# Performance work log

Measured on AMD Instinct MI355X. Metric: run time of the kernel, lower is better.

The kernel has to match this reference:

```python
import jax, jax.numpy as jnp
import numpy as np

B, S, H = 32, 2048, 1024
A = 1024  # attention_hidden_size
EPS = 1e-5


def setup_inputs() -> dict:
    key = jax.random.key(0)
    ks = jax.random.split(key, 16)
    sc_h = 1.0 / np.sqrt(H)
    sc_a = 1.0 / np.sqrt(A)
    sc_2h = 1.0 / np.sqrt(2 * H)
    return {
        "seq_states": jax.random.normal(ks[0], (B, S, H), jnp.float32),
        "q_state": jax.random.normal(ks[1], (B, H), jnp.float32),
        "Wk": jax.random.uniform(ks[2], (H, A), jnp.float32, -sc_h, sc_h),
        "bk": jax.random.uniform(ks[3], (A,), jnp.float32, -sc_h, sc_h),
        "Wq": jax.random.uniform(ks[4], (H, A), jnp.float32, -sc_h, sc_h),
        "bq": jax.random.uniform(ks[5], (A,), jnp.float32, -sc_h, sc_h),
        "Wg": jax.random.uniform(ks[6], (A, A), jnp.float32, -sc_a, sc_a),
        "bg": jax.random.uniform(ks[7], (A,), jnp.float32, -sc_a, sc_a),
        "Ws": jax.random.uniform(ks[8], (A, 1), jnp.float32, -sc_a, sc_a),
        "bs": jax.random.uniform(ks[9], (1,), jnp.float32, -sc_a, sc_a),
        "Wo": jax.random.uniform(ks[10], (2 * H, H), jnp.float32, -sc_2h, sc_2h),
        "bo": jax.random.uniform(ks[11], (H,), jnp.float32, -sc_2h, sc_2h),
        "gamma": jnp.ones((H,), jnp.float32),
        "beta": jnp.zeros((H,), jnp.float32),
    }


def reference(seq_states, q_state, Wk, bk, Wq, bq, Wg, bg, Ws, bs, Wo, bo, gamma, beta):
    keys = jnp.einsum("bsh,ha->bsa", seq_states, Wk) + bk          # [B,S,A]
    query = (q_state @ Wq + bq)[:, None, :]                          # [B,1,A]
    alignment = jnp.tanh(keys + query)                               # [B,S,A]
    gate = jax.nn.sigmoid(jnp.einsum("bsa,ac->bsc", alignment, Wg) + bg)
    gated = alignment * gate                                         # dropout p=0.0 -> identity
    scores = jnp.einsum("bsa,ao->bso", gated, Ws)[..., 0] + bs[0]    # [B,S]
    weights = jax.nn.softmax(scores, axis=1)                         # [B,S]
    context = jnp.einsum("bs,bsh->bh", weights, seq_states)          # [B,H]
    fused_in = jnp.concatenate([context, q_state], axis=-1)          # [B,2H]
    pre = fused_in @ Wo + bo + q_state                               # residual
    mu = jnp.mean(pre, axis=-1, keepdims=True)
    var = jnp.var(pre, axis=-1, keepdims=True)
    fused = (pre - mu) * jax.lax.rsqrt(var + EPS) * gamma + beta
    return (fused, weights)
```

## Files before the change

kernel.cpp:

```cpp
#include <hip/hip_runtime.h>

typedef __attribute__((ext_vector_type(8))) short bf16x8;
typedef __attribute__((ext_vector_type(8))) unsigned short ushort8;
typedef __attribute__((ext_vector_type(4))) unsigned short ushortx4;
typedef __attribute__((ext_vector_type(4))) float f32x4;

#define BM 256
#define BN 256
#define BK 64

__device__ __forceinline__ unsigned short f2bf(float f) {
  union { float f; unsigned u; } c; c.f = f;
  return (unsigned short)((c.u + 0x7fffu + ((c.u >> 16) & 1u)) >> 16);
}
__device__ __forceinline__ float bf2f(unsigned short u) {
  union { unsigned u; float f; } c; c.u = ((unsigned)u) << 16;
  return c.f;
}
__device__ __forceinline__ float fast_tanh(float x) {
  float e = __expf(2.f * x);
  return 1.f - 2.f * __builtin_amdgcn_rcpf(e + 1.f);
}
__device__ __forceinline__ float fast_sigmoid(float x) {
  return __builtin_amdgcn_rcpf(1.f + __expf(-x));
}
__device__ __forceinline__ void gload16(const void* g, void* lds) {
  __builtin_amdgcn_global_load_lds(
      (const __attribute__((address_space(1))) unsigned int*)g,
      (__attribute__((address_space(3))) unsigned int*)lds, 16, 0, 0);
}
__device__ __forceinline__ void bar() {
  asm volatile("" ::: "memory");
  __builtin_amdgcn_s_barrier();
  asm volatile("" ::: "memory");
}
__device__ __forceinline__ void sb0() { __builtin_amdgcn_sched_barrier(0); }
template <int N> __device__ __forceinline__ void vlgkm() {
  if constexpr (N == 0) asm volatile("s_waitcnt lgkmcnt(0)" ::: "memory");
  else if constexpr (N == 4) asm volatile("s_waitcnt lgkmcnt(4)" ::: "memory");
  else if constexpr (N == 8) asm volatile("s_waitcnt lgkmcnt(8)" ::: "memory");
}
template <int N> __device__ __forceinline__ void vwait() {
  if constexpr (N < 0) {
  } else if constexpr (N == 2) asm volatile("s_waitcnt vmcnt(2)" ::: "memory");
  else if constexpr (N == 0) asm volatile("s_waitcnt vmcnt(0)" ::: "memory");
}

__device__ __forceinline__ void mfma16(const bf16x8 (&a)[4], const bf16x8 (&b)[4], int ro,
                                       f32x4 (&acc)[8][4]) {
  __builtin_amdgcn_s_setprio(1);
#pragma unroll
  for (int i = 0; i < 4; ++i)
#pragma unroll
    for (int n = 0; n < 4; ++n)
      acc[ro + i][n] =
          __builtin_amdgcn_mfma_f32_16x16x32_bf16(a[i], b[n], acc[ro + i][n], 0, 0, 0);
  __builtin_amdgcn_s_setprio(0);
}

template <bool ST, bool ST4, bool RD4, int W3, int W4>
__device__ __forceinline__ void ktile(
    const char* rAk0, const char* rAk1, const char* rBk1,
    const char* rAk0n, const char* rBk0n,
    char* dAn, char* dBn,
    char* dAc,
    const unsigned short* pA0, const unsigned short* pA1,
    const unsigned short* pB0, const unsigned short* pB1,
    int kN1, int kN2,
    bf16x8 (&aX)[4], bf16x8 (&aY)[4], bf16x8 (&b0)[4], bf16x8 (&b1)[4],
    f32x4 (&acc)[8][4]) {
  bar();
#pragma unroll
  for (int i = 0; i < 4; ++i) aY[i] = *(const bf16x8*)(rAk0 + 16384 + i * 2048);
  if (ST) { gload16(pB0 + kN1, dBn); gload16(pB1 + kN1, dBn + 8192); }
  vlgkm<4>(); sb0();
  mfma16(aX, b0, 0, acc);
  bar();
#pragma unroll
  for (int i = 0; i < 4; ++i) aX[i] = *(const bf16x8*)(rAk1 + i * 2048);
#pragma unroll
  for (int n = 0; n < 4; ++n)
    b1[n] = *(const bf16x8*)(rBk1 + (n >> 1) * 16384 + (n & 1) * 2048);
  if (ST) { gload16(pB0 + 32768 + kN1, dBn + 16384); gload16(pB1 + 32768 + kN1, dBn + 16384 + 8192); }
  vlgkm<8>(); sb0();
  mfma16(aY, b0, 4, acc);
  bar();
#pragma unroll
  for (int i = 0; i < 4; ++i) aY[i] = *(const bf16x8*)(rAk1 + 16384 + i * 2048);
  if (ST) { gload16(pA0 + 65536 + kN1, dAn + 16384); gload16(pA1 + 65536 + kN1, dAn + 16384 + 8192); }
  vlgkm<4>(); sb0();
  mfma16(aX, b1, 0, acc);
  vwait<W3>();
  bar();
  if (RD4) {
#pragma unroll
    for (int i = 0; i < 4; ++i) aX[i] = *(const bf16x8*)(rAk0n + i * 2048);
#pragma unroll
    for (int n = 0; n < 4; ++n)
      b0[n] = *(const bf16x8*)(rBk0n + (n >> 1) * 16384 + (n & 1) * 2048);
  }
  if (ST4) { gload16(pA0 + kN2, dAc); gload16(pA1 + kN2, dAc + 8192); }
  if (RD4) vlgkm<8>(); else vlgkm<0>();
  sb0();
  mfma16(aY, b1, 4, acc);
  vwait<W4>();
}

#define GEMM_SETUP_AND_PIPELINE(Ag, Bg)                                                    \
  int t = threadIdx.x, lane = t & 63, wave = t >> 6;                                       \
  int wr = wave >> 2, wc = wave & 3;                                                       \
  int sl0 = ((lane >> 4) ^ (lane & 7)) * 16;                                               \
  int sl1 = (((lane >> 4) + 4) ^ (lane & 7)) * 16;                                         \
  int aLane = (wr * 64 + (lane & 15)) * 128;                                               \
  int bLane = (wc * 32 + (lane & 15)) * 128;                                               \
  const char* rA0k0 = (const char*)As0 + aLane + sl0;                                      \
  const char* rA0k1 = (const char*)As0 + aLane + sl1;                                      \
  const char* rA1k0 = (const char*)As1 + aLane + sl0;                                      \
  const char* rA1k1 = (const char*)As1 + aLane + sl1;                                      \
  const char* rB0k0 = (const char*)Bs0 + bLane + sl0;                                      \
  const char* rB0k1 = (const char*)Bs0 + bLane + sl1;                                      \
  const char* rB1k0 = (const char*)Bs1 + bLane + sl0;                                      \
  const char* rB1k1 = (const char*)Bs1 + bLane + sl1;                                      \
  char* dA0 = (char*)As0 + t * 16;                                                         \
  char* dA1 = (char*)As1 + t * 16;                                                         \
  char* dB0 = (char*)Bs0 + t * 16;                                                         \
  char* dB1 = (char*)Bs1 + t * 16;                                                         \
  int l3 = t >> 3;                                                                         \
  int sgE = ((t & 7) ^ (l3 & 7)) * 8;                                                      \
  const unsigned short* pA0 = Ag + (size_t)(m0 + l3) * 1024 + sgE;                         \
  const unsigned short* pA1 = pA0 + (size_t)128 * 1024;                                    \
  int nB0 = ((l3 >> 5) << 6) + (l3 & 31);                                                  \
  const unsigned short* pB0 = Bg + (size_t)(n0 + nB0) * 1024 + sgE;                        \
  const unsigned short* pB1 = pB0 + (size_t)128 * 1024;                                    \
  f32x4 acc[8][4] = {};                                                                    \
  bf16x8 aX[4], aY[4], b0f[4], b1f[4];                                                     \
                                         \
  gload16(pA0, dA0); gload16(pA1, dA0 + 8192);                                             \
  gload16(pB0, dB0); gload16(pB1, dB0 + 8192);                                             \
  gload16(pB0 + 32768, dB0 + 16384); gload16(pB1 + 32768, dB0 + 16384 + 8192);             \
  gload16(pA0 + 65536, dA0 + 16384); gload16(pA1 + 65536, dA0 + 16384 + 8192);             \
  vwait<2>();                                                                              \
  bar();                                                                                   \
                             \
  _Pragma("unroll") for (int i = 0; i < 4; ++i)                                            \
      aX[i] = *(const bf16x8*)(rA0k0 + i * 2048);                                          \
  _Pragma("unroll") for (int n = 0; n < 4; ++n)                                            \
      b0f[n] = *(const bf16x8*)(rB0k0 + (n >> 1) * 16384 + (n & 1) * 2048);                \
  gload16(pA0 + 64, dA1); gload16(pA1 + 64, dA1 + 8192);                                   \
  vwait<2>();                                                                              \
  _Pragma("unroll 1") for (int kt = 0; kt < 14; kt += 2) {                                 \
    ktile<true, true, true, 2, 2>(rA0k0, rA0k1, rB0k1, rA1k0, rB1k0, dA1, dB1, dA0,        \
        pA0, pA1, pB0, pB1, (kt + 1) * 64, (kt + 2) * 64, aX, aY, b0f, b1f, acc);          \
    ktile<true, true, true, 2, 2>(rA1k0, rA1k1, rB1k1, rA0k0, rB0k0, dA0, dB0, dA1,        \
        pA0, pA1, pB0, pB1, (kt + 2) * 64, (kt + 3) * 64, aX, aY, b0f, b1f, acc);          \
  }                                                                                        \
  ktile<true, false, true, 2, 0>(rA0k0, rA0k1, rB0k1, rA1k0, rB1k0, dA1, dB1, dA0,         \
      pA0, pA1, pB0, pB1, 960, 0, aX, aY, b0f, b1f, acc);                                  \
  ktile<false, false, false, -1, -1>(rA1k0, rA1k1, rB1k1, rA0k0, rB0k0, dA0, dB0, dA1,     \
      pA0, pA1, pB0, pB1, 0, 0, aX, aY, b0f, b1f, acc);

__device__ __forceinline__ void tile_coords(int bid, int& m0, int& n0, int& nt) {
  int lin = (bid & 7) * 128 + (bid >> 3);
  int mt = lin >> 2;
  nt = lin & 3;
  m0 = mt * BM;
  n0 = nt * BN;
}

__global__ __launch_bounds__(256) void prep_kernel(
    const float* __restrict__ seq, unsigned short* __restrict__ seqb,
    const float* __restrict__ Wk, const float* __restrict__ Wg,
    unsigned short* __restrict__ WkT, unsigned short* __restrict__ WgT,
    const float* __restrict__ q, const float* __restrict__ Wq,
    float* __restrict__ qp) {
  __shared__ float smem[4160];
  int bid = blockIdx.x, t = threadIdx.x;
  if (bid < 2048) {
    size_t i = ((size_t)bid * 256 + t) * 8;
    const size_t stride = (size_t)2048 * 256 * 8;
    for (; i < (size_t)67108864; i += stride) {
      f32x4 v0 = *(const f32x4*)(seq + i);
      f32x4 v1 = *(const f32x4*)(seq + i + 4);
      ushort8 o;
#pragma unroll
      for (int k = 0; k < 4; ++k) { o[k] = f2bf(v0[k]); o[k + 4] = f2bf(v1[k]); }
      *(ushort8*)(seqb + i) = o;
    }
  } else if (bid < 2560) {
    int b2 = bid - 2048;
    int mat = b2 >> 8;
    int tid = b2 & 255;
    int tr = tid >> 4, tc = tid & 15;
    const float* src = mat ? Wg : Wk;
    unsigned short* dst = mat ? WgT : WkT;
    int r0 = tr * 64, c0 = tc * 64;
    int lr = t >> 6, lc = t & 63;
#pragma unroll
    for (int i = 0; i < 16; ++i) {
      int r = i * 4 + lr;
      smem[r * 65 + lc] = src[(size_t)(r0 + r) * 1024 + c0 + lc];
    }
    __syncthreads();
#pragma unroll
    for (int i = 0; i < 16; ++i) {
      int r = i * 4 + lr;
      dst[(size_t)(c0 + r) * 1024 + r0 + lc] = f2bf(smem[lc * 65 + r]);
    }
  } else {
    int b3 = bid - 2560;
    int ac = b3 & 3, hc = b3 >> 2;
    int h0 = hc * 128;
    for (int i = t; i < 4096; i += 256) {
      int b = i >> 7, hh = i & 127;
      smem[b * 128 + hh] = q[(size_t)b * 1024 + h0 + hh];
    }
    __syncthreads();
    int a = ac * 256 + t;
    float acc[32] = {};
    for (int hh = 0; hh < 128; hh += 4) {
      float w0 = Wq[(size_t)(h0 + hh) * 1024 + a];
      float w1 = Wq[(size_t)(h0 + hh + 1) * 1024 + a];
      float w2 = Wq[(size_t)(h0 + hh + 2) * 1024 + a];
      float w3 = Wq[(size_t)(h0 + hh + 3) * 1024 + a];
#pragma unroll
      for (int b = 0; b < 32; ++b) {
        f32x4 qv = *(const f32x4*)&smem[b * 128 + hh];
        acc[b] += qv[0] * w0 + qv[1] * w1 + qv[2] * w2 + qv[3] * w3;
      }
    }
#pragma unroll
    for (int b = 0; b < 32; ++b) qp[((size_t)(hc * 32 + b)) * 1024 + a] = acc[b];
  }
}

__global__ __launch_bounds__(512, 2) void gemm1_kernel(
    const unsigned short* __restrict__ seqb, const unsigned short* __restrict__ WkT,
    const float* __restrict__ qp, const float* __restrict__ bq,
    const float* __restrict__ bk, unsigned short* __restrict__ alignb) {
  __shared__ unsigned short As0[BM * BK], Bs0[BN * BK], As1[BM * BK], Bs1[BN * BK];
  int m0, n0, nt;
  tile_coords(blockIdx.x, m0, n0, nt);
  GEMM_SETUP_AND_PIPELINE(seqb, WkT)

  int bidx = m0 >> 11;
  float qv[4];
#pragma unroll
  for (int ni = 0; ni < 4; ++ni) {
    int col = n0 + wc * 64 + ni * 16 + (lane & 15);
    float s = bq[col] + bk[col];
#pragma unroll
    for (int hc = 0; hc < 8; ++hc) s += qp[((size_t)(hc * 32 + bidx)) * 1024 + col];
    qv[ni] = s;
  }
#pragma unroll
  for (int mi = 0; mi < 8; ++mi) {
    int row0 = m0 + wr * 128 + mi * 16 + ((lane >> 4) * 4);
#pragma unroll
    for (int ni = 0; ni < 4; ++ni) {
      int col = n0 + wc * 64 + ni * 16 + (lane & 15);
#pragma unroll
      for (int j = 0; j < 4; ++j) {
        float v = fast_tanh(acc[mi][ni][j] + qv[ni]);
        alignb[(size_t)(row0 + j) * 1024 + col] = f2bf(v);
      }
    }
  }
}

__global__ __launch_bounds__(512, 2) void gemm2_kernel(
    const unsigned short* __restrict__ alignb, const unsigned short* __restrict__ WgT,
    const float* __restrict__ bg, const float* __restrict__ Ws,
    float* __restrict__ scores_part) {
  __shared__ unsigned short As0[BM * BK], Bs0[BN * BK], As1[BM * BK], Bs1[BN * BK];
  __shared__ float sred[BM * 4];
  int m0, n0, nt;
  tile_coords(blockIdx.x, m0, n0, nt);
  GEMM_SETUP_AND_PIPELINE(alignb, WgT)

#pragma unroll
  for (int mi = 0; mi < 8; ++mi) {
#pragma unroll
    for (int j = 0; j < 4; ++j) {
      int rloc = wr * 128 + mi * 16 + ((lane >> 4) * 4) + j;
      int row = m0 + rloc;
      float p = 0.f;
#pragma unroll
      for (int ni = 0; ni < 4; ++ni) {
        int col = n0 + wc * 64 + ni * 16 + (lane & 15);
        float gate = fast_sigmoid(acc[mi][ni][j] + bg[col]);
        float al = bf2f(alignb[(size_t)row * 1024 + col]);
        p += al * gate * Ws[col];
      }
      p += __shfl_xor(p, 1);
      p += __shfl_xor(p, 2);
      p += __shfl_xor(p, 4);
      p += __shfl_xor(p, 8);
      if ((lane & 15) == 0) sred[rloc * 4 + wc] = p;
    }
  }
  __syncthreads();
  if (t < 256)
    scores_part[(size_t)nt * 65536 + m0 + t] =
        sred[t * 4] + sred[t * 4 + 1] + sred[t * 4 + 2] + sred[t * 4 + 3];
}

__global__ __launch_bounds__(256) void softmax_kernel(const float* __restrict__ sp,
                                                      float* __restrict__ wout) {
  __shared__ float red[256];
  int b = blockIdx.x, t = threadIdx.x;
  float sc[8];
  float lmax = -1e30f;
#pragma unroll
  for (int i = 0; i < 8; ++i) {
    int s = i * 256 + t;
    float v = 0.f;
#pragma unroll
    for (int n = 0; n < 4; ++n) v += sp[(size_t)n * 65536 + b * 2048 + s];
    sc[i] = v;
    lmax = fmaxf(lmax, v);
  }
  red[t] = lmax;
  __syncthreads();
  for (int off = 128; off > 0; off >>= 1) {
    if (t < off) red[t] = fmaxf(red[t], red[t + off]);
    __syncthreads();
  }
  float mx = red[0];
  __syncthreads();
  float lsum = 0.f;
#pragma unroll
  for (int i = 0; i < 8; ++i) {
    sc[i] = expf(sc[i] - mx);
    lsum += sc[i];
  }
  red[t] = lsum;
  __syncthreads();
  for (int off = 128; off > 0; off >>= 1) {
    if (t < off) red[t] += red[t + off];
    __syncthreads();
  }
  float inv = 1.f / red[0];
#pragma unroll
  for (int i = 0; i < 8; ++i) wout[(size_t)b * 2048 + i * 256 + t] = sc[i] * inv;
}

__global__ __launch_bounds__(256) void context_kernel(const unsigned short* __restrict__ seqb,
                                                      const float* __restrict__ wts,
                                                      float* __restrict__ ctx_part) {
  __shared__ float wsh[128];
  int b = blockIdx.x, t = threadIdx.x, s0 = blockIdx.z * 128;
  int h0 = t * 4;
  if (t < 128) wsh[t] = wts[(size_t)b * 2048 + s0 + t];
  __syncthreads();
  float a0 = 0.f, a1 = 0.f, a2 = 0.f, a3 = 0.f;
  const unsigned short* p = seqb + ((size_t)b * 2048 + s0) * 1024 + h0;
#pragma unroll 4
  for (int s = 0; s < 128; ++s) {
    ushortx4 v = *(const ushortx4*)(p + (size_t)s * 1024);
    float w = wsh[s];
    a0 += w * bf2f(v[0]);
    a1 += w * bf2f(v[1]);
    a2 += w * bf2f(v[2]);
    a3 += w * bf2f(v[3]);
  }
  float* dst = ctx_part + (size_t)(blockIdx.z * 32 + b) * 1024 + h0;
  dst[0] = a0; dst[1] = a1; dst[2] = a2; dst[3] = a3;
}

__global__ __launch_bounds__(256) void pre_kernel(const float* __restrict__ ctx_part,
                                                  const float* __restrict__ q,
                                                  const float* __restrict__ Wo,
                                                  float* __restrict__ pre_part) {
  __shared__ float fin[32 * 128];
  int kc = blockIdx.x, hc = blockIdx.y, t = threadIdx.x;
  int k0 = kc * 128, h0 = hc * 256;
  for (int i = t; i < 4096; i += 256) {
    int b = i >> 7, kk = i & 127, k = k0 + kk;
    float f;
    if (k < 1024) {
      f = 0.f;
#pragma unroll
      for (int s = 0; s < 16; ++s) f += ctx_part[((size_t)(s * 32 + b)) * 1024 + k];
    } else {
      f = q[(size_t)b * 1024 + (k - 1024)];
    }
    fin[b * 128 + kk] = f;
  }
  __syncthreads();
  int h = h0 + t;
  float acc[32] = {};
  for (int kk = 0; kk < 128; kk += 4) {
    float w0 = Wo[(size_t)(k0 + kk) * 1024 + h];
    float w1 = Wo[(size_t)(k0 + kk + 1) * 1024 + h];
    float w2 = Wo[(size_t)(k0 + kk + 2) * 1024 + h];
    float w3 = Wo[(size_t)(k0 + kk + 3) * 1024 + h];
#pragma unroll
    for (int b = 0; b < 32; ++b) {
      f32x4 fv = *(const f32x4*)&fin[b * 128 + kk];
      acc[b] += fv[0] * w0 + fv[1] * w1 + fv[2] * w2 + fv[3] * w3;
    }
  }
#pragma unroll
  for (int b = 0; b < 32; ++b) pre_part[((size_t)(kc * 32 + b)) * 1024 + h] = acc[b];
}

__global__ __launch_bounds__(256) void ln_kernel(const float* __restrict__ pre_part,
                                                 const float* __restrict__ q,
                                                 const float* __restrict__ bo,
                                                 const float* __restrict__ gamma,
                                                 const float* __restrict__ beta,
                                                 float* __restrict__ outF) {
  __shared__ float red[256];
  int b = blockIdx.x, t = threadIdx.x;
  float v[4];
  float lsum = 0.f;
#pragma unroll
  for (int i = 0; i < 4; ++i) {
    int h = i * 256 + t;
    float x = bo[h] + q[(size_t)b * 1024 + h];
#pragma unroll
    for (int kc = 0; kc < 16; ++kc) x += pre_part[((size_t)(kc * 32 + b)) * 1024 + h];
    v[i] = x;
    lsum += x;
  }
  red[t] = lsum;
  __syncthreads();
  for (int off = 128; off > 0; off >>= 1) {
    if (t < off) red[t] += red[t + off];
    __syncthreads();
  }
  float mu = red[0] * (1.f / 1024.f);
  __syncthreads();
  float lv = 0.f;
#pragma unroll
  for (int i = 0; i < 4; ++i) {
    float d = v[i] - mu;
    lv += d * d;
  }
  red[t] = lv;
  __syncthreads();
  for (int off = 128; off > 0; off >>= 1) {
    if (t < off) red[t] += red[t + off];
    __syncthreads();
  }
  float var = red[0] * (1.f / 1024.f);
  float rs = rsqrtf(var + 1e-5f);
#pragma unroll
  for (int i = 0; i < 4; ++i) {
    int h = i * 256 + t;
    outF[(size_t)b * 1024 + h] = (v[i] - mu) * rs * gamma[h] + beta[h];
  }
}

extern "C" void kernel_launch(void* const* d_in, const int* in_sizes, int n_in,
                              void* d_out, int out_size, void* d_ws, size_t ws_size,
                              hipStream_t stream) {
  const float* seq = (const float*)d_in[0];
  const float* q = (const float*)d_in[1];
  const float* Wk = (const float*)d_in[2];
  const float* bk = (const float*)d_in[3];
  const float* Wq = (const float*)d_in[4];
  const float* bq = (const float*)d_in[5];
  const float* Wg = (const float*)d_in[6];
  const float* bg = (const float*)d_in[7];
  const float* Ws = (const float*)d_in[8];
  const float* Wo = (const float*)d_in[10];
  const float* bo = (const float*)d_in[11];
  const float* gamma = (const float*)d_in[12];
  const float* beta = (const float*)d_in[13];

  float* outF = (float*)d_out;
  float* outW = outF + 32 * 1024;

  char* ws = (char*)d_ws;
  unsigned short* alignb = (unsigned short*)ws;  ws += (size_t)134217728;
  unsigned short* seqb = (unsigned short*)ws;    ws += (size_t)134217728;
  unsigned short* WkT = (unsigned short*)ws;     ws += 2097152;
  unsigned short* WgT = (unsigned short*)ws;     ws += 2097152;
  float* qp = (float*)ws;                        ws += 1048576;
  float* scores_part = (float*)ws;               ws += 1048576;
  float* ctx_part = (float*)ws;                  ws += 2097152;
  float* pre_part = (float*)ws;                  ws += 2097152;
  if (ws_size < (size_t)(ws - (char*)d_ws)) return;

  prep_kernel<<<2592, 256, 0, stream>>>(seq, seqb, Wk, Wg, WkT, WgT, q, Wq, qp);
  gemm1_kernel<<<1024, 512, 0, stream>>>(seqb, WkT, qp, bq, bk, alignb);
  gemm2_kernel<<<1024, 512, 0, stream>>>(alignb, WgT, bg, Ws, scores_part);
  softmax_kernel<<<32, 256, 0, stream>>>(scores_part, outW);
  context_kernel<<<dim3(32, 1, 16), 256, 0, stream>>>(seqb, outW, ctx_part);
  pre_kernel<<<dim3(16, 4), 256, 0, stream>>>(ctx_part, q, Wo, pre_part);
  ln_kernel<<<32, 256, 0, stream>>>(pre_part, q, bo, gamma, beta, outF);
}
```

Measured before the change: 506.0 us.

## Replace gemm2 pipelined 256x256 tile with simple single-buffered 128x128 tile kernel

The gate GEMM kernel drops the double-buffered, software-pipelined 256x256 tile with 8 waves and uses a plain 128x128 tile with 4 waves and a single LDS buffer. Each k-step loads the tile, waits, runs the MFMAs and then synchronises. The grid grows to 4096 blocks, so score partials are split 8 ways instead of 4, and the softmax and workspace are resized to match. This gives more, smaller blocks, but loses the overlap of loads with compute and cuts data reuse per tile.

New measurement: 487.9 us. 1.04x faster.

```diff
diff --git a/kernel.cpp b/kernel.cpp
--- a/kernel.cpp
+++ b/kernel.cpp
@@ -56,6 +56,15 @@
       acc[ro + i][n] =
           __builtin_amdgcn_mfma_f32_16x16x32_bf16(a[i], b[n], acc[ro + i][n], 0, 0, 0);
   __builtin_amdgcn_s_setprio(0);
+}
+__device__ __forceinline__ void mfma16_4(const bf16x8 (&a)[4], const bf16x8 (&b)[4],
+                                         f32x4 (&acc)[4][4]) {
+#pragma unroll
+  for (int i = 0; i < 4; ++i)
+#pragma unroll
+    for (int n = 0; n < 4; ++n)
+      acc[i][n] =
+          __builtin_amdgcn_mfma_f32_16x16x32_bf16(a[i], b[n], acc[i][n], 0, 0, 0);
 }
 
 template <bool ST, bool ST4, bool RD4, int W3, int W4>
@@ -134,14 +143,12 @@
   const unsigned short* pB1 = pB0 + (size_t)128 * 1024;                                    \
   f32x4 acc[8][4] = {};                                                                    \
   bf16x8 aX[4], aY[4], b0f[4], b1f[4];                                                     \
-                                         \
   gload16(pA0, dA0); gload16(pA1, dA0 + 8192);                                             \
   gload16(pB0, dB0); gload16(pB1, dB0 + 8192);                                             \
   gload16(pB0 + 32768, dB0 + 16384); gload16(pB1 + 32768, dB0 + 16384 + 8192);             \
   gload16(pA0 + 65536, dA0 + 16384); gload16(pA1 + 65536, dA0 + 16384 + 8192);             \
   vwait<2>();                                                                              \
   bar();                                                                                   \
-                             \
   _Pragma("unroll") for (int i = 0; i < 4; ++i)                                            \
       aX[i] = *(const bf16x8*)(rA0k0 + i * 2048);                                          \
   _Pragma("unroll") for (int n = 0; n < 4; ++n)                                            \
@@ -267,21 +274,61 @@
   }
 }
 
-__global__ __launch_bounds__(512, 2) void gemm2_kernel(
+__global__ __launch_bounds__(256, 2) void gemm2_kernel(
     const unsigned short* __restrict__ alignb, const unsigned short* __restrict__ WgT,
     const float* __restrict__ bg, const float* __restrict__ Ws,
     float* __restrict__ scores_part) {
-  __shared__ unsigned short As0[BM * BK], Bs0[BN * BK], As1[BM * BK], Bs1[BN * BK];
-  __shared__ float sred[BM * 4];
-  int m0, n0, nt;
-  tile_coords(blockIdx.x, m0, n0, nt);
-  GEMM_SETUP_AND_PIPELINE(alignb, WgT)
-
-#pragma unroll
-  for (int mi = 0; mi < 8; ++mi) {
+  __shared__ unsigned short As[128 * 64];
+  __shared__ unsigned short Bs[128 * 64];
+  __shared__ float sred[128 * 2];
+  int lin = (blockIdx.x & 7) * 512 + (blockIdx.x >> 3);
+  int mt = lin >> 3, nt = lin & 7;
+  int m0 = mt * 128, n0 = nt * 128;
+  int t = threadIdx.x, lane = t & 63, wave = t >> 6;
+  int wr = wave >> 1, wc = wave & 1;
+  int sl0 = ((lane >> 4) ^ (lane & 7)) * 16;
+  int sl1 = (((lane >> 4) + 4) ^ (lane & 7)) * 16;
+  const char* rAk0 = (const char*)As + (wr * 64 + (lane & 15)) * 128 + sl0;
+  const char* rAk1 = (const char*)As + (wr * 64 + (lane & 15)) * 128 + sl1;
+  const char* rBk0 = (const char*)Bs + (wc * 64 + (lane & 15)) * 128 + sl0;
+  const char* rBk1 = (const char*)Bs + (wc * 64 + (lane & 15)) * 128 + sl1;
+  int l3 = t >> 3;
+  int sgE = ((t & 7) ^ (l3 & 7)) * 8;
+  const unsigned short* pA = alignb + (size_t)(m0 + l3) * 1024 + sgE;
+  const unsigned short* pB = WgT + (size_t)(n0 + l3) * 1024 + sgE;
+  char* dA = (char*)As + t * 16;
+  char* dB = (char*)Bs + t * 16;
+  f32x4 acc[4][4] = {};
+#pragma unroll 1
+  for (int kt = 0; kt < 16; ++kt) {
+    int k0 = kt * 64;
+#pragma unroll
+    for (int r = 0; r < 4; ++r) {
+      gload16(pA + (size_t)(r * 32) * 1024 + k0, dA + r * 4096);
+      gload16(pB + (size_t)(r * 32) * 1024 + k0, dB + r * 4096);
+    }
+    vwait<0>();
+    bar();
+    {
+      bf16x8 a[4], b[4];
+#pragma unroll
+      for (int i = 0; i < 4; ++i) a[i] = *(const bf16x8*)(rAk0 + i * 2048);
+#pragma unroll
+      for (int n = 0; n < 4; ++n) b[n] = *(const bf16x8*)(rBk0 + n * 2048);
+      mfma16_4(a, b, acc);
+#pragma unroll
+      for (int i = 0; i < 4; ++i) a[i] = *(const bf16x8*)(rAk1 + i * 2048);
+#pragma unroll
+      for (int n = 0; n < 4; ++n) b[n] = *(const bf16x8*)(rBk1 + n * 2048);
+      mfma16_4(a, b, acc);
+    }
+    bar();
+  }
+#pragma unroll
+  for (int mi = 0; mi < 4; ++mi) {
 #pragma unroll
     for (int j = 0; j < 4; ++j) {
-      int rloc = wr * 128 + mi * 16 + ((lane >> 4) * 4) + j;
+      int rloc = wr * 64 + mi * 16 + ((lane >> 4) * 4) + j;
       int row = m0 + rloc;
       float p = 0.f;
 #pragma unroll
@@ -295,13 +342,11 @@
       p += __shfl_xor(p, 2);
       p += __shfl_xor(p, 4);
       p += __shfl_xor(p, 8);
-      if ((lane & 15) == 0) sred[rloc * 4 + wc] = p;
-    }
-  }
-  __syncthreads();
-  if (t < 256)
-    scores_part[(size_t)nt * 65536 + m0 + t] =
-        sred[t * 4] + sred[t * 4 + 1] + sred[t * 4 + 2] + sred[t * 4 + 3];
+      if ((lane & 15) == 0) sred[rloc * 2 + wc] = p;
+    }
+  }
+  __syncthreads();
+  if (t < 128) scores_part[(size_t)nt * 65536 + m0 + t] = sred[t * 2] + sred[t * 2 + 1];
 }
 
 __global__ __launch_bounds__(256) void softmax_kernel(const float* __restrict__ sp,
@@ -315,7 +360,7 @@
     int s = i * 256 + t;
     float v = 0.f;
 #pragma unroll
-    for (int n = 0; n < 4; ++n) v += sp[(size_t)n * 65536 + b * 2048 + s];
+    for (int n = 0; n < 8; ++n) v += sp[(size_t)n * 65536 + b * 2048 + s];
     sc[i] = v;
     lmax = fmaxf(lmax, v);
   }
@@ -478,14 +523,14 @@
   unsigned short* WkT = (unsigned short*)ws;     ws += 2097152;
   unsigned short* WgT = (unsigned short*)ws;     ws += 2097152;
   float* qp = (float*)ws;                        ws += 1048576;
-  float* scores_part = (float*)ws;               ws += 1048576;
+  float* scores_part = (float*)ws;               ws += 2097152;
   float* ctx_part = (float*)ws;                  ws += 2097152;
   float* pre_part = (float*)ws;                  ws += 2097152;
   if (ws_size < (size_t)(ws - (char*)d_ws)) return;
 
   prep_kernel<<<2592, 256, 0, stream>>>(seq, seqb, Wk, Wg, WkT, WgT, q, Wq, qp);
   gemm1_kernel<<<1024, 512, 0, stream>>>(seqb, WkT, qp, bq, bk, alignb);
-  gemm2_kernel<<<1024, 512, 0, stream>>>(alignb, WgT, bg, Ws, scores_part);
+  gemm2_kernel<<<4096, 256, 0, stream>>>(alignb, WgT, bg, Ws, scores_part);
   softmax_kernel<<<32, 256, 0, stream>>>(scores_part, outW);
   context_kernel<<<dim3(32, 1, 16), 256, 0, stream>>>(seqb, outW, ctx_part);
   pre_kernel<<<dim3(16, 4), 256, 0, stream>>>(ctx_part, q, Wo, pre_part);
```
